# Performance work log

Hardware: AMD Instinct MI355X
Metric: run time of the kernel (lower is better)

The kernel has to match this reference:

```python
import jax, jax.numpy as jnp
import numpy as np

N_NODES = 50000
N_EDGES = 800000
IN_F = 256
OUT_F = 64


def setup_inputs() -> dict:
    key = jax.random.key(0)
    k1, k2, k3, k4, k5 = jax.random.split(key, 5)
    x = jax.random.normal(k1, (N_NODES, IN_F), dtype=jnp.float32)
    # xavier-uniform-like init for weight
    limit = float(np.sqrt(6.0 / (IN_F + OUT_F)))
    weight = jax.random.uniform(k2, (IN_F, OUT_F), dtype=jnp.float32, minval=-limit, maxval=limit)
    bias = jnp.zeros((1, OUT_F), dtype=jnp.float32)
    edge_weight = jax.random.uniform(k3, (N_EDGES,), dtype=jnp.float32)
    edge_src = jax.random.randint(k4, (N_EDGES,), 0, N_NODES, dtype=jnp.int32)
    edge_dst = jax.random.randint(k5, (N_EDGES,), 0, N_NODES, dtype=jnp.int32)
    return {"x": x, "weight": weight, "bias": bias,
            "edge_weight": edge_weight, "edge_src": edge_src, "edge_dst": edge_dst}


def reference(x, weight, bias, edge_weight, edge_src, edge_dst):
    # in_features (256) > out_features (64): transform first, then propagate.
    h = x @ weight                                  # [N, out]
    # spmm with COO adjacency: out[dst] += w_e * h[src]
    msgs = h[edge_src] * edge_weight[:, None]       # [E, out]
    out = jax.ops.segment_sum(msgs, edge_dst, num_segments=x.shape[0])  # [N, out]
    return out + bias
```

## Files before the change

### kernel.cpp

```cpp
#include <hip/hip_runtime.h>
#include <hip/hip_bf16.h>

#define N_NODES 50000
#define N_EDGES 800000
#define IN_F 256
#define OUT_F 64

#define CAP 64

typedef __attribute__((ext_vector_type(8))) short short8;
typedef __attribute__((ext_vector_type(4))) float f32x4;

static __device__ __forceinline__ ushort f2bf(float v) {
    __hip_bfloat16 b = __float2bfloat16(v);
    return *(ushort*)&b;
}

__global__ __launch_bounds__(256) void gc_mid(const float* __restrict__ x,
                                              const float* __restrict__ W,
                                              ushort* __restrict__ h,
                                              const int* __restrict__ esrc,
                                              const int* __restrict__ edst,
                                              const float* __restrict__ ew,
                                              int* __restrict__ cnt,
                                              unsigned int* __restrict__ slots) {
    __shared__ ushort xs[32 * 264];
    const int t = threadIdx.x;
    const int bid = blockIdx.x;
    const int r3 = bid % 3;

    if (r3 == 2) {
        const int e = (bid / 3) * 1024 + t * 4;
        if (e < N_EDGES) {
            const int4 s4 = *(const int4*)(esrc + e);
            const int4 d4 = *(const int4*)(edst + e);
            const float4 w4 = *(const float4*)(ew + e);

            const int p0 = atomicAdd(&cnt[d4.x], 1);
            const int p1 = atomicAdd(&cnt[d4.y], 1);
            const int p2 = atomicAdd(&cnt[d4.z], 1);
            const int p3 = atomicAdd(&cnt[d4.w], 1);

            if (p0 < CAP)
                slots[(size_t)d4.x * CAP + p0] =
                    ((unsigned)f2bf(w4.x) << 16) | (unsigned)(s4.x & 0xFFFF);
            if (p1 < CAP)
                slots[(size_t)d4.y * CAP + p1] =
                    ((unsigned)f2bf(w4.y) << 16) | (unsigned)(s4.y & 0xFFFF);
            if (p2 < CAP)
                slots[(size_t)d4.z * CAP + p2] =
                    ((unsigned)f2bf(w4.z) << 16) | (unsigned)(s4.z & 0xFFFF);
            if (p3 < CAP)
                slots[(size_t)d4.w * CAP + p3] =
                    ((unsigned)f2bf(w4.w) << 16) | (unsigned)(s4.w & 0xFFFF);
        }
        return;
    }

    const int g = bid - bid / 3;
    const int nbase = g * 32;
    if (nbase >= N_NODES) return;

    {
#pragma unroll
        for (int i = 0; i < 8; ++i) {
            const int idx = t + i * 256;
            const int node = idx >> 6;
            const int c4 = idx & 63;
            int gnode = nbase + node;
            if (gnode >= N_NODES) gnode = N_NODES - 1;
            const float4 v = ((const float4*)x)[(size_t)gnode * 64 + c4];
            ushort4 b;
            b.x = f2bf(v.x); b.y = f2bf(v.y); b.z = f2bf(v.z); b.w = f2bf(v.w);
            *(ushort4*)&xs[node * 264 + c4 * 4] = b;
        }
    }

    const int s = t >> 6;
    const int lane = t & 63;
    const int m = lane & 15;
    const int quad = lane >> 4;

    short8 bfrag[8];
    {
        const float* __restrict__ wp = W + (size_t)(quad * 8) * OUT_F + s * 16 + m;
#pragma unroll
        for (int kk = 0; kk < 8; ++kk) {
            short8 bf;
#pragma unroll
            for (int j = 0; j < 8; ++j)
                bf[j] = (short)f2bf(wp[(size_t)(kk * 32 + j) * OUT_F]);
            bfrag[kk] = bf;
        }
    }

    __syncthreads();

    f32x4 acc0 = {0.f, 0.f, 0.f, 0.f};
    f32x4 acc1 = {0.f, 0.f, 0.f, 0.f};
#pragma unroll
    for (int kk = 0; kk < 8; ++kk) {
        const short8 a0 = *(const short8*)&xs[m * 264 + kk * 32 + quad * 8];
        const short8 a1 = *(const short8*)&xs[(16 + m) * 264 + kk * 32 + quad * 8];
        acc0 = __builtin_amdgcn_mfma_f32_16x16x32_bf16(a0, bfrag[kk], acc0, 0, 0, 0);
        acc1 = __builtin_amdgcn_mfma_f32_16x16x32_bf16(a1, bfrag[kk], acc1, 0, 0, 0);
    }

#pragma unroll
    for (int r = 0; r < 4; ++r) {
        const int row0 = nbase + quad * 4 + r;
        const int row1 = row0 + 16;
        if (row0 < N_NODES) h[(size_t)row0 * OUT_F + s * 16 + m] = f2bf(acc0[r]);
        if (row1 < N_NODES) h[(size_t)row1 * OUT_F + s * 16 + m] = f2bf(acc1[r]);
    }
}

__global__ __launch_bounds__(256) void gc_gather(const ushort* __restrict__ h,
                                                 const unsigned int* __restrict__ slots,
                                                 const int* __restrict__ cnt,
                                                 const float* __restrict__ bias,
                                                 float* __restrict__ out) {
    const int wid = __builtin_amdgcn_readfirstlane(
        (int)((blockIdx.x * 256 + threadIdx.x) >> 6));
    const int f = threadIdx.x & 63;
    const int d0 = wid * 8;
    if (d0 >= N_NODES) return;

    const int4 ca = *(const int4*)(cnt + d0);
    const int4 cb = *(const int4*)(cnt + d0 + 4);
    const int dg0 = min(ca.x, CAP), dg1 = min(ca.y, CAP);
    const int dg2 = min(ca.z, CAP), dg3 = min(ca.w, CAP);
    const int dg4 = min(cb.x, CAP), dg5 = min(cb.y, CAP);
    const int dg6 = min(cb.z, CAP), dg7 = min(cb.w, CAP);
    const int mdeg = max(max(max(dg0, dg1), max(dg2, dg3)),
                         max(max(dg4, dg5), max(dg6, dg7)));

    const unsigned sw0 = (f < dg0) ? slots[(size_t)(d0 + 0) * CAP + f] : 0u;
    const unsigned sw1 = (f < dg1) ? slots[(size_t)(d0 + 1) * CAP + f] : 0u;
    const unsigned sw2 = (f < dg2) ? slots[(size_t)(d0 + 2) * CAP + f] : 0u;
    const unsigned sw3 = (f < dg3) ? slots[(size_t)(d0 + 3) * CAP + f] : 0u;
    const unsigned sw4 = (f < dg4) ? slots[(size_t)(d0 + 4) * CAP + f] : 0u;
    const unsigned sw5 = (f < dg5) ? slots[(size_t)(d0 + 5) * CAP + f] : 0u;
    const unsigned sw6 = (f < dg6) ? slots[(size_t)(d0 + 6) * CAP + f] : 0u;
    const unsigned sw7 = (f < dg7) ? slots[(size_t)(d0 + 7) * CAP + f] : 0u;

    const float b = bias[f];
    float a0 = b, a1 = b, a2 = b, a3 = b, a4 = b, a5 = b, a6 = b, a7 = b;

    const ushort* __restrict__ hf = h + f;

#define ROWLD(sw, l) \
    hf[(size_t)((unsigned)__builtin_amdgcn_readlane((int)(sw), (l)) & 0xFFFFu) * OUT_F]
#define WBITS(sw, l) \
    __uint_as_float((unsigned)__builtin_amdgcn_readlane((int)(sw), (l)) & 0xFFFF0000u)

    for (int i0 = 0; i0 < mdeg; i0 += 8) {
        unsigned hv0[8], hv1[8], hv2[8], hv3[8], hv4[8], hv5[8], hv6[8], hv7[8];
#pragma unroll
        for (int j = 0; j < 8; ++j) {
            const int l = i0 + j;
            hv0[j] = ROWLD(sw0, l);
            hv1[j] = ROWLD(sw1, l);
            hv2[j] = ROWLD(sw2, l);
            hv3[j] = ROWLD(sw3, l);
            hv4[j] = ROWLD(sw4, l);
            hv5[j] = ROWLD(sw5, l);
            hv6[j] = ROWLD(sw6, l);
            hv7[j] = ROWLD(sw7, l);
        }
#pragma unroll
        for (int j = 0; j < 8; ++j) {
            const int l = i0 + j;
            a0 += WBITS(sw0, l) * __uint_as_float(hv0[j] << 16);
            a1 += WBITS(sw1, l) * __uint_as_float(hv1[j] << 16);
            a2 += WBITS(sw2, l) * __uint_as_float(hv2[j] << 16);
            a3 += WBITS(sw3, l) * __uint_as_float(hv3[j] << 16);
            a4 += WBITS(sw4, l) * __uint_as_float(hv4[j] << 16);
            a5 += WBITS(sw5, l) * __uint_as_float(hv5[j] << 16);
            a6 += WBITS(sw6, l) * __uint_as_float(hv6[j] << 16);
            a7 += WBITS(sw7, l) * __uint_as_float(hv7[j] << 16);
        }
    }
#undef ROWLD
#undef WBITS

    out[(size_t)(d0 + 0) * OUT_F + f] = a0;
    out[(size_t)(d0 + 1) * OUT_F + f] = a1;
    out[(size_t)(d0 + 2) * OUT_F + f] = a2;
    out[(size_t)(d0 + 3) * OUT_F + f] = a3;
    out[(size_t)(d0 + 4) * OUT_F + f] = a4;
    out[(size_t)(d0 + 5) * OUT_F + f] = a5;
    out[(size_t)(d0 + 6) * OUT_F + f] = a6;
    out[(size_t)(d0 + 7) * OUT_F + f] = a7;
}

extern "C" void kernel_launch(void* const* d_in, const int* in_sizes, int n_in,
                              void* d_out, int out_size, void* d_ws, size_t ws_size,
                              hipStream_t stream) {
    const float* x    = (const float*)d_in[0];
    const float* W    = (const float*)d_in[1];
    const float* bias = (const float*)d_in[2];
    const float* ew   = (const float*)d_in[3];
    const int* src    = (const int*)d_in[4];
    const int* dst    = (const int*)d_in[5];
    float* out = (float*)d_out;

    char* ws = (char*)d_ws;
    ushort* h           = (ushort*)ws;
    int* cnt            = (int*)(ws + 6400000);
    unsigned int* slots = (unsigned int*)(ws + 6600000);

    hipMemsetAsync(cnt, 0, N_NODES * sizeof(int), stream);

    gc_mid<<<2346, 256, 0, stream>>>(x, W, h, src, dst, ew, cnt, slots);

    gc_gather<<<1563, 256, 0, stream>>>(h, slots, cnt, bias, out);
}
```

Before: 155.9 us.

## Split fused GEMM/edge-placement kernel and pre-swizzle bf16 weights in prep kernel

Replaces the hipMemset with a prep kernel that zeroes the per-node counters and also converts W once into bf16 MFMA B-fragment layout. The fused kernel, which interleaved edge-placement blocks with GEMM blocks, is split into separate place and gemm kernels. Each GEMM block now loads pre-swizzled short8 fragments instead of doing strided fp32 loads and converting them. This costs an extra launch and serialises placement before the GEMM, giving up the overlap the fused kernel had.

```diff
diff --git a/kernel.cpp b/kernel.cpp
--- a/kernel.cpp
+++ b/kernel.cpp
@@ -16,50 +16,60 @@
     return *(ushort*)&b;
 }
 
-__global__ __launch_bounds__(256) void gc_mid(const float* __restrict__ x,
-                                              const float* __restrict__ W,
-                                              ushort* __restrict__ h,
-                                              const int* __restrict__ esrc,
-                                              const int* __restrict__ edst,
-                                              const float* __restrict__ ew,
-                                              int* __restrict__ cnt,
-                                              unsigned int* __restrict__ slots) {
+__global__ __launch_bounds__(256) void gc_prep(const float* __restrict__ W,
+                                               ushort* __restrict__ Wb,
+                                               int* __restrict__ cnt) {
+    const int g = blockIdx.x * 256 + threadIdx.x;
+    if (g < N_NODES) cnt[g] = 0;
+    if (g < 2048) {
+        const int s = g >> 9;
+        const int kk = (g >> 6) & 7;
+        const int lane = g & 63;
+        const int n = s * 16 + (lane & 15);
+        const int kb = kk * 32 + (lane >> 4) * 8;
+#pragma unroll
+        for (int j = 0; j < 8; ++j)
+            Wb[(size_t)g * 8 + j] = f2bf(W[(kb + j) * OUT_F + n]);
+    }
+}
+
+__global__ __launch_bounds__(256) void gc_place(const int* __restrict__ esrc,
+                                                const int* __restrict__ edst,
+                                                const float* __restrict__ ew,
+                                                int* __restrict__ cnt,
+                                                unsigned int* __restrict__ slots) {
+    const int e = blockIdx.x * 1024 + threadIdx.x * 4;
+    if (e < N_EDGES) {
+        const int4 s4 = *(const int4*)(esrc + e);
+        const int4 d4 = *(const int4*)(edst + e);
+        const float4 w4 = *(const float4*)(ew + e);
+
+        const int p0 = atomicAdd(&cnt[d4.x], 1);
+        const int p1 = atomicAdd(&cnt[d4.y], 1);
+        const int p2 = atomicAdd(&cnt[d4.z], 1);
+        const int p3 = atomicAdd(&cnt[d4.w], 1);
+
+        if (p0 < CAP)
+            slots[(size_t)d4.x * CAP + p0] =
+                ((unsigned)f2bf(w4.x) << 16) | (unsigned)(s4.x & 0xFFFF);
+        if (p1 < CAP)
+            slots[(size_t)d4.y * CAP + p1] =
+                ((unsigned)f2bf(w4.y) << 16) | (unsigned)(s4.y & 0xFFFF);
+        if (p2 < CAP)
+            slots[(size_t)d4.z * CAP + p2] =
+                ((unsigned)f2bf(w4.z) << 16) | (unsigned)(s4.z & 0xFFFF);
+        if (p3 < CAP)
+            slots[(size_t)d4.w * CAP + p3] =
+                ((unsigned)f2bf(w4.w) << 16) | (unsigned)(s4.w & 0xFFFF);
+    }
+}
+
+__global__ __launch_bounds__(256) void gc_gemm(const float* __restrict__ x,
+                                               const ushort* __restrict__ Wb,
+                                               ushort* __restrict__ h) {
     __shared__ ushort xs[32 * 264];
     const int t = threadIdx.x;
-    const int bid = blockIdx.x;
-    const int r3 = bid % 3;
-
-    if (r3 == 2) {
-        const int e = (bid / 3) * 1024 + t * 4;
-        if (e < N_EDGES) {
-            const int4 s4 = *(const int4*)(esrc + e);
-            const int4 d4 = *(const int4*)(edst + e);
-            const float4 w4 = *(const float4*)(ew + e);
-
-            const int p0 = atomicAdd(&cnt[d4.x], 1);
-            const int p1 = atomicAdd(&cnt[d4.y], 1);
-            const int p2 = atomicAdd(&cnt[d4.z], 1);
-            const int p3 = atomicAdd(&cnt[d4.w], 1);
-
-            if (p0 < CAP)
-                slots[(size_t)d4.x * CAP + p0] =
-                    ((unsigned)f2bf(w4.x) << 16) | (unsigned)(s4.x & 0xFFFF);
-            if (p1 < CAP)
-                slots[(size_t)d4.y * CAP + p1] =
-                    ((unsigned)f2bf(w4.y) << 16) | (unsigned)(s4.y & 0xFFFF);
-            if (p2 < CAP)
-                slots[(size_t)d4.z * CAP + p2] =
-                    ((unsigned)f2bf(w4.z) << 16) | (unsigned)(s4.z & 0xFFFF);
-            if (p3 < CAP)
-                slots[(size_t)d4.w * CAP + p3] =
-                    ((unsigned)f2bf(w4.w) << 16) | (unsigned)(s4.w & 0xFFFF);
-        }
-        return;
-    }
-
-    const int g = bid - bid / 3;
-    const int nbase = g * 32;
-    if (nbase >= N_NODES) return;
+    const int nbase = blockIdx.x * 32;
 
     {
 #pragma unroll
@@ -82,17 +92,9 @@
     const int quad = lane >> 4;
 
     short8 bfrag[8];
-    {
-        const float* __restrict__ wp = W + (size_t)(quad * 8) * OUT_F + s * 16 + m;
-#pragma unroll
-        for (int kk = 0; kk < 8; ++kk) {
-            short8 bf;
-#pragma unroll
-            for (int j = 0; j < 8; ++j)
-                bf[j] = (short)f2bf(wp[(size_t)(kk * 32 + j) * OUT_F]);
-            bfrag[kk] = bf;
-        }
-    }
+#pragma unroll
+    for (int kk = 0; kk < 8; ++kk)
+        bfrag[kk] = *(const short8*)(Wb + ((size_t)(s * 8 + kk) * 64 + lane) * 8);
 
     __syncthreads();
 
@@ -209,10 +211,10 @@
     ushort* h           = (ushort*)ws;
     int* cnt            = (int*)(ws + 6400000);
     unsigned int* slots = (unsigned int*)(ws + 6600000);
-
-    hipMemsetAsync(cnt, 0, N_NODES * sizeof(int), stream);
-
-    gc_mid<<<2346, 256, 0, stream>>>(x, W, h, src, dst, ew, cnt, slots);
-
+    ushort* Wb          = (ushort*)(ws + 19400000);
+
+    gc_prep<<<196, 256, 0, stream>>>(W, Wb, cnt);
+    gc_place<<<782, 256, 0, stream>>>(src, dst, ew, cnt, slots);
+    gc_gemm<<<1563, 256, 0, stream>>>(x, Wb, h);
     gc_gather<<<1563, 256, 0, stream>>>(h, slots, cnt, bias, out);
 }
```

Measured after the change: 170.8 us. 9.5% more time.
